# Optimization experiments

Hardware: AMD Instinct MI355X
Metric: run time of the kernel (lower is better)

Reference implementation:

```python
import jax, jax.numpy as jnp
import numpy as np

B = 65536
NEGO = 48        # num_ego_obs
NADO = 24        # num_ado_obs
NTEAMS, TSIZE = 2, 3
NA = NTEAMS * TSIZE          # num_agents = 6
NADOAG = NA - 1              # 5 ado agents
E = 256                      # embed_dims[-1]
H = 4                        # attention heads
AD = 256 // H                # attend_dim = 64


def setup_inputs() -> dict:
    key = jax.random.key(0)
    ks = jax.random.split(key, 16)
    w = lambda k, shape: jax.random.normal(k, shape, jnp.float32) * 0.05
    return {
        "observations": jax.random.normal(ks[0], (B, NEGO + NADOAG * NADO), jnp.float32),
        # ego encoder: Linear(48,256)+LeakyReLU, Linear(256,256)+LeakyReLU
        "ego_w0": w(ks[1], (NEGO, E)), "ego_b0": jnp.zeros((E,), jnp.float32),
        "ego_w1": w(ks[2], (E, E)),    "ego_b1": jnp.zeros((E,), jnp.float32),
        # ado encoder: Linear(25,256)+LeakyReLU, Linear(256,256)+LeakyReLU
        "ado_w0": w(ks[3], (NADO + 1, E)), "ado_b0": jnp.zeros((E,), jnp.float32),
        "ado_w1": w(ks[4], (E, E)),        "ado_b1": jnp.zeros((E,), jnp.float32),
        # per-head extractors stacked on a leading head axis
        "key_w": w(ks[5], (H, E, AD)),   # no bias
        "sel_w": w(ks[6], (H, E, AD)),   # no bias
        "lat_w": w(ks[7], (H, E, AD)), "lat_b": jnp.zeros((H, AD), jnp.float32),
        # projection: Linear(256, 64)
        "proj_w": w(ks[8], (H * AD, AD)), "proj_b": jnp.zeros((AD,), jnp.float32),
    }


def reference(observations, ego_w0, ego_b0, ego_w1, ego_b1,
              ado_w0, ado_b0, ado_w1, ado_b1,
              key_w, sel_w, lat_w, lat_b, proj_w, proj_b):
    lrelu = jax.nn.leaky_relu  # slope 0.01, matches nn.LeakyReLU()
    obs_ego = observations[:, :NEGO]                              # [B, 48]
    obs_ado = observations[:, NEGO:NEGO + NADOAG * NADO]          # [B, 120]
    team_ids = jnp.asarray([t for t in range(NTEAMS) for _ in range(TSIZE)],
                           jnp.float32)                           # [6]

    # ego latent [B, E]
    ego = lrelu(lrelu(obs_ego @ ego_w0 + ego_b0) @ ego_w1 + ego_b1)

    # ado_ag_obs[..., ado_id::5] == reshape(B, NADO, 5)[:, :, ado_id]
    ado_obs = obs_ado.reshape(-1, NADO, NADOAG).transpose(0, 2, 1)  # [B, 5, 24]
    tid = jnp.broadcast_to(team_ids[1:NA][None, :, None],
                           (ado_obs.shape[0], NADOAG, 1))           # [B, 5, 1]
    ado_in = jnp.concatenate([ado_obs, tid], axis=-1)               # [B, 5, 25]
    ado = lrelu(lrelu(ado_in @ ado_w0 + ado_b0) @ ado_w1 + ado_b1)  # [B, 5, E]

    slct = jnp.einsum('be,hed->bhd', ego, sel_w)                    # [B, H, AD]
    keys = jnp.einsum('bne,hed->bnhd', ado, key_w)                  # [B, 5, H, AD]
    lats = lrelu(jnp.einsum('bne,hed->bnhd', ado, lat_w) + lat_b)   # [B, 5, H, AD]

    logits = jnp.einsum('bhd,bnhd->bhn', slct, keys) / jnp.sqrt(jnp.float32(AD))
    attn = jax.nn.softmax(logits, axis=-1)                          # [B, H, 5]
    agg = jnp.einsum('bhn,bnhd->bhd', attn, lats).reshape(-1, H * AD)  # heads concat in order
    proj = agg @ proj_w + proj_b                                    # [B, 64]
    return jnp.concatenate([obs_ego, proj], axis=-1)                # [B, 112]
```

## Files before the change

kernel.cpp:

```cpp
#include <hip/hip_runtime.h>
#include <hip/hip_bf16.h>


typedef __bf16 bf16x8 __attribute__((ext_vector_type(8)));
typedef __bf16 bf16x4 __attribute__((ext_vector_type(4)));
typedef float  f32x4  __attribute__((ext_vector_type(4)));

#define OFF_EGO0 0
#define OFF_EGO1 16384
#define OFF_ADO0 81920
#define OFF_ADO1 90112
#define OFF_SEL  155648
#define OFF_KEY  221184
#define OFF_LAT  286720
#define OFF_PROJ 352256
#define WS_ELEMS 368640

__global__ __launch_bounds__(256) void prep_weights(
    const float* __restrict__ ew0, const float* __restrict__ ew1,
    const float* __restrict__ aw0, const float* __restrict__ aw1,
    const float* __restrict__ keyw, const float* __restrict__ selw,
    const float* __restrict__ latw, const float* __restrict__ projw,
    __bf16* __restrict__ ws)
{
  int i = blockIdx.x * 256 + threadIdx.x;
  if (i >= WS_ELEMS) return;
  float v;
  if (i < OFF_EGO1)      { int j=i;          int c=j>>6, k=j&63;  v = (k<48) ? ew0[k*256+c] : 0.f; }
  else if (i < OFF_ADO0) { int j=i-OFF_EGO1; int c=j>>8, k=j&255; v = ew1[k*256+c]; }
  else if (i < OFF_ADO1) { int j=i-OFF_ADO0; int c=j>>5, k=j&31;  v = (k<25) ? aw0[k*256+c] : 0.f; }
  else if (i < OFF_SEL)  { int j=i-OFF_ADO1; int c=j>>8, k=j&255; v = aw1[k*256+c]; }
  else if (i < OFF_KEY)  { int j=i-OFF_SEL;  int c=j>>8, k=j&255; v = selw[(c>>6)*16384 + k*64 + (c&63)]; }
  else if (i < OFF_LAT)  { int j=i-OFF_KEY;  int c=j>>8, k=j&255; v = keyw[(c>>6)*16384 + k*64 + (c&63)]; }
  else if (i < OFF_PROJ) { int j=i-OFF_LAT;  int c=j>>8, k=j&255; v = latw[(c>>6)*16384 + k*64 + (c&63)]; }
  else                   { int j=i-OFF_PROJ; int c=j>>8, k=j&255; v = projw[k*64+c]; }
  ws[i] = (__bf16)v;
}

__device__ __forceinline__ bf16x8 lds_loadA(const __bf16* base, int row, int kByte, int rowBytes) {
  int off = (row * rowBytes + kByte) ^ ((row & 7) << 4);
  return *reinterpret_cast<const bf16x8*>(reinterpret_cast<const char*>(base) + off);
}
__device__ __forceinline__ void lds_store_bf16(__bf16* base, int row, int col, __bf16 v) {
  int off = (row * 512 + col * 2) ^ ((row & 7) << 4);
  *reinterpret_cast<__bf16*>(reinterpret_cast<char*>(base) + off) = v;
}

#define P_ADO2   0
#define P_EGOIN  0
#define P_EGOH1  2048
#define P_ADOIN  24576
#define P_EGOH2  40960
#define P_PROJIN 40960
#define P_H1     49152
#define P_OUT    73728
#define POOL_BYTES 77824

template<int KP, int R, bool ACT>
__device__ __forceinline__ void gemm_block(const __bf16* __restrict__ sA, int aRow0,
                                           __bf16* __restrict__ sC, int cRow0,
                                           const __bf16* __restrict__ WT,
                                           const float* __restrict__ bias,
                                           int w, int lr, int lg)
{
  constexpr int NKB = KP / 32;
  #pragma unroll
  for (int cth = 0; cth < 2; ++cth) {
    f32x4 acc[R][2];
    #pragma unroll
    for (int t = 0; t < R; ++t) {
      acc[t][0] = f32x4{0.f,0.f,0.f,0.f};
      acc[t][1] = f32x4{0.f,0.f,0.f,0.f};
    }
    #pragma unroll
    for (int kb = 0; kb < NKB; ++kb) {
      bf16x8 af[R];
      #pragma unroll
      for (int t = 0; t < R; ++t)
        af[t] = lds_loadA(sA, aRow0 + t*16 + lr, kb*64 + lg*16, KP*2);
      #pragma unroll
      for (int c2 = 0; c2 < 2; ++c2) {
        const int col = w*64 + (cth*2 + c2)*16 + lr;
        bf16x8 bfr = *reinterpret_cast<const bf16x8*>(WT + col*KP + kb*32 + lg*8);
        #pragma unroll
        for (int t = 0; t < R; ++t)
          acc[t][c2] = __builtin_amdgcn_mfma_f32_16x16x32_bf16(af[t], bfr, acc[t][c2], 0, 0, 0);
      }
    }
    #pragma unroll
    for (int c2 = 0; c2 < 2; ++c2) {
      const int col = w*64 + (cth*2 + c2)*16 + lr;
      const float bv = bias[col];
      #pragma unroll
      for (int t = 0; t < R; ++t) {
        #pragma unroll
        for (int e = 0; e < 4; ++e) {
          float x = acc[t][c2][e] + bv;
          if (ACT) x = x > 0.f ? x : 0.01f * x;
          lds_store_bf16(sC, cRow0 + t*16 + lg*4 + e, col, (__bf16)x);
        }
      }
    }
  }
}

__global__ __launch_bounds__(256) void fused_kernel(
    const float* __restrict__ obs,
    const float* __restrict__ eb0, const float* __restrict__ eb1,
    const float* __restrict__ ab0, const float* __restrict__ ab1,
    const float* __restrict__ latb, const float* __restrict__ projb,
    const __bf16* __restrict__ ws,
    float* __restrict__ out)
{
  const int tid = threadIdx.x;
  const int w  = tid >> 6;
  const int l  = tid & 63;
  const int lr = l & 15;
  const int lg = l >> 4;
  const int b0 = blockIdx.x * 16;

  __shared__ __align__(16) char pool[POOL_BYTES];
  __bf16* sEgoIn = reinterpret_cast<__bf16*>(pool + P_EGOIN);
  __bf16* sEgoH1 = reinterpret_cast<__bf16*>(pool + P_EGOH1);
  __bf16* sAdoIn = reinterpret_cast<__bf16*>(pool + P_ADOIN);
  __bf16* sEgoH2 = reinterpret_cast<__bf16*>(pool + P_EGOH2);
  __bf16* sProj  = reinterpret_cast<__bf16*>(pool + P_PROJIN);
  __bf16* sAdo2  = reinterpret_cast<__bf16*>(pool + P_ADO2);
  __bf16* sH1    = reinterpret_cast<__bf16*>(pool + P_H1);
  float*  sOutF  = reinterpret_cast<float*>(pool + P_OUT);

  {
    if (tid < 192) {
      int row = tid / 12, c4 = tid % 12;
      f32x4 v = *reinterpret_cast<const f32x4*>(obs + (size_t)(b0+row)*168 + c4*4);
      __builtin_nontemporal_store(v,
          reinterpret_cast<f32x4*>(out + (size_t)(b0+row)*112 + c4*4));
      bf16x4 bv = { (__bf16)v[0], (__bf16)v[1], (__bf16)v[2], (__bf16)v[3] };
      int off = (row*128 + c4*8) ^ ((row&7)<<4);
      *reinterpret_cast<bf16x4*>(reinterpret_cast<char*>(sEgoIn) + off) = bv;
    } else {
      int t = tid - 192;
      int row = t >> 2, ch = t & 3;
      bf16x4 z = {};
      int off = (row*128 + 96 + ch*8) ^ ((row&7)<<4);
      *reinterpret_cast<bf16x4*>(reinterpret_cast<char*>(sEgoIn) + off) = z;
    }
    if (tid < 240) {
      int ldsrow = tid / 3, p = tid % 3;
      int n = ldsrow >> 4, r = ldsrow & 15;
      const float* orow = obs + (size_t)(b0+r)*168 + 48;
      bf16x8 v;
      #pragma unroll
      for (int j = 0; j < 8; ++j) v[j] = (__bf16)orow[(p*8+j)*5 + n];
      int off = (ldsrow*64 + p*16) ^ ((ldsrow&7)<<4);
      *reinterpret_cast<bf16x8*>(reinterpret_cast<char*>(sAdoIn) + off) = v;
    }
    if (tid < 80) {
      int n = tid >> 4;
      bf16x8 v = {};
      v[0] = (__bf16)((n >= 2) ? 1.0f : 0.0f);
      int off = (tid*64 + 48) ^ ((tid&7)<<4);
      *reinterpret_cast<bf16x8*>(reinterpret_cast<char*>(sAdoIn) + off) = v;
    }
  }
  __syncthreads();

  gemm_block<64, 1, true>(sEgoIn, 0, sEgoH1, 0, ws + OFF_EGO0, eb0, w, lr, lg);
  gemm_block<32, 3, true>(sAdoIn, 0, sH1,    0, ws + OFF_ADO0, ab0, w, lr, lg);
  __syncthreads();

  gemm_block<256, 1, true>(sEgoH1, 0, sEgoH2, 0, ws + OFF_EGO1, eb1, w, lr, lg);
  __syncthreads();

  f32x4 slct[4];
  {
    const __bf16* WT = ws + OFF_SEL;
    #pragma unroll
    for (int ct = 0; ct < 4; ++ct) slct[ct] = f32x4{0.f,0.f,0.f,0.f};
    #pragma unroll
    for (int kb = 0; kb < 8; ++kb) {
      bf16x8 af = lds_loadA(sEgoH2, lr, kb*64 + lg*16, 512);
      #pragma unroll
      for (int ct = 0; ct < 4; ++ct) {
        bf16x8 bfr = *reinterpret_cast<const bf16x8*>(WT + (w*64+ct*16+lr)*256 + kb*32 + lg*8);
        slct[ct] = __builtin_amdgcn_mfma_f32_16x16x32_bf16(af, bfr, slct[ct], 0, 0, 0);
      }
    }
  }
  gemm_block<256, 3, true>(sH1, 0, sAdo2, 0, ws + OFF_ADO1, ab1, w, lr, lg);
  __syncthreads();

  gemm_block<32, 2, true>(sAdoIn, 48, sH1, 0, ws + OFF_ADO0, ab0, w, lr, lg);
  __syncthreads();

  gemm_block<256, 2, true>(sH1, 0, sAdo2, 48, ws + OFF_ADO1, ab1, w, lr, lg);
  __syncthreads();

  f32x4 part[5];
  #pragma unroll
  for (int n = 0; n < 5; ++n) part[n] = f32x4{0.f,0.f,0.f,0.f};
  {
    const __bf16* WK = ws + OFF_KEY;
    #pragma unroll
    for (int cth = 0; cth < 2; ++cth) {
      f32x4 kacc[5][2];
      #pragma unroll
      for (int n = 0; n < 5; ++n) {
        kacc[n][0] = f32x4{0.f,0.f,0.f,0.f};
        kacc[n][1] = f32x4{0.f,0.f,0.f,0.f};
      }
      #pragma unroll
      for (int kb = 0; kb < 8; ++kb) {
        bf16x8 af[5];
        #pragma unroll
        for (int n = 0; n < 5; ++n)
          af[n] = lds_loadA(sAdo2, n*16 + lr, kb*64 + lg*16, 512);
        #pragma unroll
        for (int c2 = 0; c2 < 2; ++c2) {
          const int col = w*64 + (cth*2 + c2)*16 + lr;
          bf16x8 bk = *reinterpret_cast<const bf16x8*>(WK + col*256 + kb*32 + lg*8);
          #pragma unroll
          for (int n = 0; n < 5; ++n)
            kacc[n][c2] = __builtin_amdgcn_mfma_f32_16x16x32_bf16(af[n], bk, kacc[n][c2], 0, 0, 0);
        }
      }
      #pragma unroll
      for (int c2 = 0; c2 < 2; ++c2)
        #pragma unroll
        for (int n = 0; n < 5; ++n)
          part[n] += kacc[n][c2] * slct[cth*2 + c2];
    }
  }
  #pragma unroll
  for (int n = 0; n < 5; ++n) {
    #pragma unroll
    for (int m = 1; m < 16; m <<= 1) {
      part[n][0] += __shfl_xor(part[n][0], m);
      part[n][1] += __shfl_xor(part[n][1], m);
      part[n][2] += __shfl_xor(part[n][2], m);
      part[n][3] += __shfl_xor(part[n][3], m);
    }
  }
  f32x4 p[5];
  {
    #pragma unroll
    for (int n = 0; n < 5; ++n) part[n] *= 0.125f;
    f32x4 mx = part[0];
    #pragma unroll
    for (int n = 1; n < 5; ++n)
      #pragma unroll
      for (int e = 0; e < 4; ++e) mx[e] = fmaxf(mx[e], part[n][e]);
    f32x4 s = f32x4{0.f,0.f,0.f,0.f};
    #pragma unroll
    for (int n = 0; n < 5; ++n) {
      #pragma unroll
      for (int e = 0; e < 4; ++e) p[n][e] = __expf(part[n][e] - mx[e]);
      s += p[n];
    }
    f32x4 inv;
    #pragma unroll
    for (int e = 0; e < 4; ++e) inv[e] = 1.0f / s[e];
    #pragma unroll
    for (int n = 0; n < 5; ++n) p[n] *= inv;
  }
  f32x4 agg[4];
  #pragma unroll
  for (int ct = 0; ct < 4; ++ct) agg[ct] = f32x4{0.f,0.f,0.f,0.f};
  {
    const __bf16* WL = ws + OFF_LAT;
    #pragma unroll
    for (int cth = 0; cth < 2; ++cth) {
      f32x4 lacc[5][2];
      #pragma unroll
      for (int n = 0; n < 5; ++n) {
        lacc[n][0] = f32x4{0.f,0.f,0.f,0.f};
        lacc[n][1] = f32x4{0.f,0.f,0.f,0.f};
      }
      #pragma unroll
      for (int kb = 0; kb < 8; ++kb) {
        bf16x8 af[5];
        #pragma unroll
        for (int n = 0; n < 5; ++n)
          af[n] = lds_loadA(sAdo2, n*16 + lr, kb*64 + lg*16, 512);
        #pragma unroll
        for (int c2 = 0; c2 < 2; ++c2) {
          const int col = w*64 + (cth*2 + c2)*16 + lr;
          bf16x8 bl = *reinterpret_cast<const bf16x8*>(WL + col*256 + kb*32 + lg*8);
          #pragma unroll
          for (int n = 0; n < 5; ++n)
            lacc[n][c2] = __builtin_amdgcn_mfma_f32_16x16x32_bf16(af[n], bl, lacc[n][c2], 0, 0, 0);
        }
      }
      #pragma unroll
      for (int c2 = 0; c2 < 2; ++c2) {
        const int ct = cth*2 + c2;
        const float lb = latb[w*64 + ct*16 + lr];
        #pragma unroll
        for (int n = 0; n < 5; ++n) {
          #pragma unroll
          for (int e = 0; e < 4; ++e) {
            float x = lacc[n][c2][e] + lb;
            x = x > 0.f ? x : 0.01f * x;
            agg[ct][e] += p[n][e] * x;
          }
        }
      }
    }
  }
  #pragma unroll
  for (int ct = 0; ct < 4; ++ct)
    #pragma unroll
    for (int e = 0; e < 4; ++e)
      lds_store_bf16(sProj, lg*4 + e, w*64 + ct*16 + lr, (__bf16)agg[ct][e]);
  __syncthreads();

  {
    const __bf16* WT = ws + OFF_PROJ;
    f32x4 pacc = f32x4{0.f,0.f,0.f,0.f};
    #pragma unroll
    for (int kb = 0; kb < 8; ++kb) {
      bf16x8 af = lds_loadA(sProj, lr, kb*64 + lg*16, 512);
      bf16x8 bfr = *reinterpret_cast<const bf16x8*>(WT + (w*16+lr)*256 + kb*32 + lg*8);
      pacc = __builtin_amdgcn_mfma_f32_16x16x32_bf16(af, bfr, pacc, 0, 0, 0);
    }
    const float pb = projb[w*16 + lr];
    #pragma unroll
    for (int e = 0; e < 4; ++e)
      sOutF[(lg*4 + e)*64 + w*16 + lr] = pacc[e] + pb;
  }
  __syncthreads();

  {
    int row = tid >> 4, q = tid & 15;
    f32x4 v = *reinterpret_cast<const f32x4*>(sOutF + row*64 + q*4);
    __builtin_nontemporal_store(v,
        reinterpret_cast<f32x4*>(out + (size_t)(b0+row)*112 + 48 + q*4));
  }
}

extern "C" void kernel_launch(void* const* d_in, const int* in_sizes, int n_in,
                              void* d_out, int out_size, void* d_ws, size_t ws_size,
                              hipStream_t stream) {
  const float* obs   = (const float*)d_in[0];
  const float* ew0   = (const float*)d_in[1];
  const float* eb0   = (const float*)d_in[2];
  const float* ew1   = (const float*)d_in[3];
  const float* eb1   = (const float*)d_in[4];
  const float* aw0   = (const float*)d_in[5];
  const float* ab0   = (const float*)d_in[6];
  const float* aw1   = (const float*)d_in[7];
  const float* ab1   = (const float*)d_in[8];
  const float* keyw  = (const float*)d_in[9];
  const float* selw  = (const float*)d_in[10];
  const float* latw  = (const float*)d_in[11];
  const float* latb  = (const float*)d_in[12];
  const float* projw = (const float*)d_in[13];
  const float* projb = (const float*)d_in[14];
  __bf16* ws = (__bf16*)d_ws;
  float* out = (float*)d_out;

  prep_weights<<<dim3((WS_ELEMS + 255)/256), dim3(256), 0, stream>>>(
      ew0, ew1, aw0, aw1, keyw, selw, latw, projw, ws);
  fused_kernel<<<dim3(65536/16), dim3(256), 0, stream>>>(
      obs, eb0, eb1, ab0, ab1, latb, projb, ws, out);
}
```

Measured before the change: 489.1 us.

## Double waves per block, split columns per wave, stage observations in LDS

The fused kernel now launches 512 threads (8 waves) per 16-row tile, and each wave computes 32 output columns instead of 64 in every GEMM stage. Because one attention head now spans two waves, partial logits are exchanged through LDS with an extra barrier before the softmax. Observation rows are first loaded into LDS with coalesced vector loads, replacing the strided global gathers for the ado inputs. The aim is more waves in flight to hide latency and fewer weight fragments per wave. In exchange, every wave still reads all A fragments from LDS, so LDS traffic roughly doubles, and the kernel adds barriers plus idle waves in the final projection and store.

```diff
diff --git a/kernel.cpp b/kernel.cpp
--- a/kernel.cpp
+++ b/kernel.cpp
@@ -53,6 +53,7 @@
 #define P_EGOH2  40960
 #define P_PROJIN 40960
 #define P_H1     49152
+#define P_OBSRAW 49152
 #define P_OUT    73728
 #define POOL_BYTES 77824
 
@@ -64,47 +65,44 @@
                                            int w, int lr, int lg)
 {
   constexpr int NKB = KP / 32;
-  #pragma unroll
-  for (int cth = 0; cth < 2; ++cth) {
-    f32x4 acc[R][2];
+  f32x4 acc[R][2];
+  #pragma unroll
+  for (int t = 0; t < R; ++t) {
+    acc[t][0] = f32x4{0.f,0.f,0.f,0.f};
+    acc[t][1] = f32x4{0.f,0.f,0.f,0.f};
+  }
+  #pragma unroll
+  for (int kb = 0; kb < NKB; ++kb) {
+    bf16x8 af[R];
+    #pragma unroll
+    for (int t = 0; t < R; ++t)
+      af[t] = lds_loadA(sA, aRow0 + t*16 + lr, kb*64 + lg*16, KP*2);
+    #pragma unroll
+    for (int c2 = 0; c2 < 2; ++c2) {
+      const int col = w*32 + c2*16 + lr;
+      bf16x8 bfr = *reinterpret_cast<const bf16x8*>(WT + col*KP + kb*32 + lg*8);
+      #pragma unroll
+      for (int t = 0; t < R; ++t)
+        acc[t][c2] = __builtin_amdgcn_mfma_f32_16x16x32_bf16(af[t], bfr, acc[t][c2], 0, 0, 0);
+    }
+  }
+  #pragma unroll
+  for (int c2 = 0; c2 < 2; ++c2) {
+    const int col = w*32 + c2*16 + lr;
+    const float bv = bias[col];
     #pragma unroll
     for (int t = 0; t < R; ++t) {
-      acc[t][0] = f32x4{0.f,0.f,0.f,0.f};
-      acc[t][1] = f32x4{0.f,0.f,0.f,0.f};
-    }
-    #pragma unroll
-    for (int kb = 0; kb < NKB; ++kb) {
-      bf16x8 af[R];
-      #pragma unroll
-      for (int t = 0; t < R; ++t)
-        af[t] = lds_loadA(sA, aRow0 + t*16 + lr, kb*64 + lg*16, KP*2);
-      #pragma unroll
-      for (int c2 = 0; c2 < 2; ++c2) {
-        const int col = w*64 + (cth*2 + c2)*16 + lr;
-        bf16x8 bfr = *reinterpret_cast<const bf16x8*>(WT + col*KP + kb*32 + lg*8);
-        #pragma unroll
-        for (int t = 0; t < R; ++t)
-          acc[t][c2] = __builtin_amdgcn_mfma_f32_16x16x32_bf16(af[t], bfr, acc[t][c2], 0, 0, 0);
-      }
-    }
-    #pragma unroll
-    for (int c2 = 0; c2 < 2; ++c2) {
-      const int col = w*64 + (cth*2 + c2)*16 + lr;
-      const float bv = bias[col];
-      #pragma unroll
-      for (int t = 0; t < R; ++t) {
-        #pragma unroll
-        for (int e = 0; e < 4; ++e) {
-          float x = acc[t][c2][e] + bv;
-          if (ACT) x = x > 0.f ? x : 0.01f * x;
-          lds_store_bf16(sC, cRow0 + t*16 + lg*4 + e, col, (__bf16)x);
-        }
-      }
-    }
-  }
-}
-
-__global__ __launch_bounds__(256) void fused_kernel(
+      #pragma unroll
+      for (int e = 0; e < 4; ++e) {
+        float x = acc[t][c2][e] + bv;
+        if (ACT) x = x > 0.f ? x : 0.01f * x;
+        lds_store_bf16(sC, cRow0 + t*16 + lg*4 + e, col, (__bf16)x);
+      }
+    }
+  }
+}
+
+__global__ __launch_bounds__(512, 4) void fused_kernel(
     const float* __restrict__ obs,
     const float* __restrict__ eb0, const float* __restrict__ eb1,
     const float* __restrict__ ab0, const float* __restrict__ ab1,
@@ -127,39 +125,55 @@
   __bf16* sProj  = reinterpret_cast<__bf16*>(pool + P_PROJIN);
   __bf16* sAdo2  = reinterpret_cast<__bf16*>(pool + P_ADO2);
   __bf16* sH1    = reinterpret_cast<__bf16*>(pool + P_H1);
+  float*  sObsF  = reinterpret_cast<float*>(pool + P_OBSRAW);
+  float*  sLogF  = reinterpret_cast<float*>(pool + P_OUT);
   float*  sOutF  = reinterpret_cast<float*>(pool + P_OUT);
+
+  {
+    const f32x4* o4 = reinterpret_cast<const f32x4*>(obs);
+    #pragma unroll
+    for (int idx = tid; idx < 672; idx += 512) {
+      int row = idx / 42, c4 = idx % 42;
+      f32x4 v = o4[(size_t)(b0+row)*42 + c4];
+      *reinterpret_cast<f32x4*>(sObsF + row*168 + c4*4) = v;
+      if (c4 < 12)
+        __builtin_nontemporal_store(v,
+            reinterpret_cast<f32x4*>(out + (size_t)(b0+row)*112 + c4*4));
+    }
+  }
+  __syncthreads();
 
   {
     if (tid < 192) {
       int row = tid / 12, c4 = tid % 12;
-      f32x4 v = *reinterpret_cast<const f32x4*>(obs + (size_t)(b0+row)*168 + c4*4);
-      __builtin_nontemporal_store(v,
-          reinterpret_cast<f32x4*>(out + (size_t)(b0+row)*112 + c4*4));
+      f32x4 v = *reinterpret_cast<const f32x4*>(sObsF + row*168 + c4*4);
       bf16x4 bv = { (__bf16)v[0], (__bf16)v[1], (__bf16)v[2], (__bf16)v[3] };
       int off = (row*128 + c4*8) ^ ((row&7)<<4);
       *reinterpret_cast<bf16x4*>(reinterpret_cast<char*>(sEgoIn) + off) = bv;
-    } else {
+    } else if (tid < 256) {
       int t = tid - 192;
       int row = t >> 2, ch = t & 3;
       bf16x4 z = {};
       int off = (row*128 + 96 + ch*8) ^ ((row&7)<<4);
       *reinterpret_cast<bf16x4*>(reinterpret_cast<char*>(sEgoIn) + off) = z;
     }
-    if (tid < 240) {
-      int ldsrow = tid / 3, p = tid % 3;
+    if (tid >= 256 && tid < 496) {
+      int t = tid - 256;
+      int ldsrow = t / 3, p = t % 3;
       int n = ldsrow >> 4, r = ldsrow & 15;
-      const float* orow = obs + (size_t)(b0+r)*168 + 48;
+      const float* orow = sObsF + r*168 + 48;
       bf16x8 v;
       #pragma unroll
       for (int j = 0; j < 8; ++j) v[j] = (__bf16)orow[(p*8+j)*5 + n];
       int off = (ldsrow*64 + p*16) ^ ((ldsrow&7)<<4);
       *reinterpret_cast<bf16x8*>(reinterpret_cast<char*>(sAdoIn) + off) = v;
     }
-    if (tid < 80) {
-      int n = tid >> 4;
+    if (tid >= 432) {
+      int t = tid - 432;
+      int n = t >> 4;
       bf16x8 v = {};
       v[0] = (__bf16)((n >= 2) ? 1.0f : 0.0f);
-      int off = (tid*64 + 48) ^ ((tid&7)<<4);
+      int off = (t*64 + 48) ^ ((t&7)<<4);
       *reinterpret_cast<bf16x8*>(reinterpret_cast<char*>(sAdoIn) + off) = v;
     }
   }
@@ -172,20 +186,22 @@
   gemm_block<256, 1, true>(sEgoH1, 0, sEgoH2, 0, ws + OFF_EGO1, eb1, w, lr, lg);
   __syncthreads();
 
-  f32x4 slct[4];
+  f32x4 slct[2];
   {
     const __bf16* WT = ws + OFF_SEL;
-    #pragma unroll
-    for (int ct = 0; ct < 4; ++ct) slct[ct] = f32x4{0.f,0.f,0.f,0.f};
+    slct[0] = f32x4{0.f,0.f,0.f,0.f};
+    slct[1] = f32x4{0.f,0.f,0.f,0.f};
     #pragma unroll
     for (int kb = 0; kb < 8; ++kb) {
       bf16x8 af = lds_loadA(sEgoH2, lr, kb*64 + lg*16, 512);
       #pragma unroll
-      for (int ct = 0; ct < 4; ++ct) {
-        bf16x8 bfr = *reinterpret_cast<const bf16x8*>(WT + (w*64+ct*16+lr)*256 + kb*32 + lg*8);
-        slct[ct] = __builtin_amdgcn_mfma_f32_16x16x32_bf16(af, bfr, slct[ct], 0, 0, 0);
-      }
-    }
+      for (int c2 = 0; c2 < 2; ++c2) {
+        bf16x8 bfr = *reinterpret_cast<const bf16x8*>(WT + (w*32+c2*16+lr)*256 + kb*32 + lg*8);
+        slct[c2] = __builtin_amdgcn_mfma_f32_16x16x32_bf16(af, bfr, slct[c2], 0, 0, 0);
+      }
+    }
+    slct[0] *= 0.125f;
+    slct[1] *= 0.125f;
   }
   gemm_block<256, 3, true>(sH1, 0, sAdo2, 0, ws + OFF_ADO1, ab1, w, lr, lg);
   __syncthreads();
@@ -202,33 +218,24 @@
   {
     const __bf16* WK = ws + OFF_KEY;
     #pragma unroll
-    for (int cth = 0; cth < 2; ++cth) {
-      f32x4 kacc[5][2];
-      #pragma unroll
-      for (int n = 0; n < 5; ++n) {
-        kacc[n][0] = f32x4{0.f,0.f,0.f,0.f};
-        kacc[n][1] = f32x4{0.f,0.f,0.f,0.f};
-      }
+    for (int c2 = 0; c2 < 2; ++c2) {
+      f32x4 kacc[5];
+      #pragma unroll
+      for (int n = 0; n < 5; ++n) kacc[n] = f32x4{0.f,0.f,0.f,0.f};
+      const int col = w*32 + c2*16 + lr;
       #pragma unroll
       for (int kb = 0; kb < 8; ++kb) {
         bf16x8 af[5];
         #pragma unroll
         for (int n = 0; n < 5; ++n)
           af[n] = lds_loadA(sAdo2, n*16 + lr, kb*64 + lg*16, 512);
-        #pragma unroll
-        for (int c2 = 0; c2 < 2; ++c2) {
-          const int col = w*64 + (cth*2 + c2)*16 + lr;
-          bf16x8 bk = *reinterpret_cast<const bf16x8*>(WK + col*256 + kb*32 + lg*8);
-          #pragma unroll
-          for (int n = 0; n < 5; ++n)
-            kacc[n][c2] = __builtin_amdgcn_mfma_f32_16x16x32_bf16(af[n], bk, kacc[n][c2], 0, 0, 0);
-        }
-      }
-      #pragma unroll
-      for (int c2 = 0; c2 < 2; ++c2)
+        bf16x8 bk = *reinterpret_cast<const bf16x8*>(WK + col*256 + kb*32 + lg*8);
         #pragma unroll
         for (int n = 0; n < 5; ++n)
-          part[n] += kacc[n][c2] * slct[cth*2 + c2];
+          kacc[n] = __builtin_amdgcn_mfma_f32_16x16x32_bf16(af[n], bk, kacc[n], 0, 0, 0);
+      }
+      #pragma unroll
+      for (int n = 0; n < 5; ++n) part[n] += kacc[n] * slct[c2];
     }
   }
   #pragma unroll
@@ -241,20 +248,28 @@
       part[n][3] += __shfl_xor(part[n][3], m);
     }
   }
+  #pragma unroll
+  for (int n = 0; n < 5; ++n)
+    if (lr == n)
+      *reinterpret_cast<f32x4*>(sLogF + (w*5 + n)*16 + lg*4) = part[n];
+  __syncthreads();
   f32x4 p[5];
   {
-    #pragma unroll
-    for (int n = 0; n < 5; ++n) part[n] *= 0.125f;
-    f32x4 mx = part[0];
+    f32x4 lt[5];
+    #pragma unroll
+    for (int n = 0; n < 5; ++n)
+      lt[n] = *reinterpret_cast<const f32x4*>(sLogF + (w*5 + n)*16 + lg*4)
+            + *reinterpret_cast<const f32x4*>(sLogF + ((w^1)*5 + n)*16 + lg*4);
+    f32x4 mx = lt[0];
     #pragma unroll
     for (int n = 1; n < 5; ++n)
       #pragma unroll
-      for (int e = 0; e < 4; ++e) mx[e] = fmaxf(mx[e], part[n][e]);
+      for (int e = 0; e < 4; ++e) mx[e] = fmaxf(mx[e], lt[n][e]);
     f32x4 s = f32x4{0.f,0.f,0.f,0.f};
     #pragma unroll
     for (int n = 0; n < 5; ++n) {
       #pragma unroll
-      for (int e = 0; e < 4; ++e) p[n][e] = __expf(part[n][e] - mx[e]);
+      for (int e = 0; e < 4; ++e) p[n][e] = __expf(lt[n][e] - mx[e]);
       s += p[n];
     }
     f32x4 inv;
@@ -263,58 +278,48 @@
     #pragma unroll
     for (int n = 0; n < 5; ++n) p[n] *= inv;
   }
-  f32x4 agg[4];
-  #pragma unroll
-  for (int ct = 0; ct < 4; ++ct) agg[ct] = f32x4{0.f,0.f,0.f,0.f};
+  f32x4 agg[2];
+  agg[0] = f32x4{0.f,0.f,0.f,0.f};
+  agg[1] = f32x4{0.f,0.f,0.f,0.f};
   {
     const __bf16* WL = ws + OFF_LAT;
     #pragma unroll
-    for (int cth = 0; cth < 2; ++cth) {
-      f32x4 lacc[5][2];
-      #pragma unroll
-      for (int n = 0; n < 5; ++n) {
-        lacc[n][0] = f32x4{0.f,0.f,0.f,0.f};
-        lacc[n][1] = f32x4{0.f,0.f,0.f,0.f};
-      }
+    for (int c2 = 0; c2 < 2; ++c2) {
+      f32x4 lacc[5];
+      #pragma unroll
+      for (int n = 0; n < 5; ++n) lacc[n] = f32x4{0.f,0.f,0.f,0.f};
+      const int col = w*32 + c2*16 + lr;
       #pragma unroll
       for (int kb = 0; kb < 8; ++kb) {
         bf16x8 af[5];
         #pragma unroll
         for (int n = 0; n < 5; ++n)
           af[n] = lds_loadA(sAdo2, n*16 + lr, kb*64 + lg*16, 512);
-        #pragma unroll
-        for (int c2 = 0; c2 < 2; ++c2) {
-          const int col = w*64 + (cth*2 + c2)*16 + lr;
-          bf16x8 bl = *reinterpret_cast<const bf16x8*>(WL + col*256 + kb*32 + lg*8);
-          #pragma unroll
-          for (int n = 0; n < 5; ++n)
-            lacc[n][c2] = __builtin_amdgcn_mfma_f32_16x16x32_bf16(af[n], bl, lacc[n][c2], 0, 0, 0);
+        bf16x8 bl = *reinterpret_cast<const bf16x8*>(WL + col*256 + kb*32 + lg*8);
+        #pragma unroll
+        for (int n = 0; n < 5; ++n)
+          lacc[n] = __builtin_amdgcn_mfma_f32_16x16x32_bf16(af[n], bl, lacc[n], 0, 0, 0);
+      }
+      const float lb = latb[col];
+      #pragma unroll
+      for (int n = 0; n < 5; ++n) {
+        #pragma unroll
+        for (int e = 0; e < 4; ++e) {
+          float x = lacc[n][e] + lb;
+          x = x > 0.f ? x : 0.01f * x;
+          agg[c2][e] += p[n][e] * x;
         }
       }
-      #pragma unroll
-      for (int c2 = 0; c2 < 2; ++c2) {
-        const int ct = cth*2 + c2;
-        const float lb = latb[w*64 + ct*16 + lr];
-        #pragma unroll
-        for (int n = 0; n < 5; ++n) {
-          #pragma unroll
-          for (int e = 0; e < 4; ++e) {
-            float x = lacc[n][c2][e] + lb;
-            x = x > 0.f ? x : 0.01f * x;
-            agg[ct][e] += p[n][e] * x;
-          }
-        }
-      }
-    }
-  }
-  #pragma unroll
-  for (int ct = 0; ct < 4; ++ct)
+    }
+  }
+  #pragma unroll
+  for (int c2 = 0; c2 < 2; ++c2)
     #pragma unroll
     for (int e = 0; e < 4; ++e)
-      lds_store_bf16(sProj, lg*4 + e, w*64 + ct*16 + lr, (__bf16)agg[ct][e]);
-  __syncthreads();
-
-  {
+      lds_store_bf16(sProj, lg*4 + e, w*32 + c2*16 + lr, (__bf16)agg[c2][e]);
+  __syncthreads();
+
+  if (w < 4) {
     const __bf16* WT = ws + OFF_PROJ;
     f32x4 pacc = f32x4{0.f,0.f,0.f,0.f};
     #pragma unroll
@@ -330,7 +335,7 @@
   }
   __syncthreads();
 
-  {
+  if (tid < 256) {
     int row = tid >> 4, q = tid & 15;
     f32x4 v = *reinterpret_cast<const f32x4*>(sOutF + row*64 + q*4);
     __builtin_nontemporal_store(v,
@@ -361,6 +366,6 @@
 
   prep_weights<<<dim3((WS_ELEMS + 255)/256), dim3(256), 0, stream>>>(
       ew0, ew1, aw0, aw1, keyw, selw, latw, projw, ws);
-  fused_kernel<<<dim3(65536/16), dim3(256), 0, stream>>>(
+  fused_kernel<<<dim3(65536/16), dim3(512), 0, stream>>>(
       obs, eb0, eb1, ab0, ab1, latb, projb, ws, out);
 }
```

New measurement: 457.7 us. 1.07x faster.

## Shrink LDS pool with in-place ado GEMMs to raise occupancy

Applied to the files above, without the earlier changes.

Reorganizes shared-memory use so the second ado layer runs in place over its input, with a barrier between the accumulate and writeback phases, which cuts the LDS pool from about 76KB to 40KB. It also sets launch_bounds to 4 blocks per CU, stages the raw observation tile into LDS with coalesced vector loads instead of strided global gathers, and folds the 1/sqrt(d) scale into the selector. The gemm helper now keeps four column tiles of accumulators live, which raises register pressure, and it adds extra block-wide barriers.

```diff
diff --git a/kernel.cpp b/kernel.cpp
--- a/kernel.cpp
+++ b/kernel.cpp
@@ -46,65 +46,61 @@
   *reinterpret_cast<__bf16*>(reinterpret_cast<char*>(base) + off) = v;
 }
 
-#define P_ADO2   0
 #define P_EGOIN  0
 #define P_EGOH1  2048
-#define P_ADOIN  24576
-#define P_EGOH2  40960
-#define P_PROJIN 40960
-#define P_H1     49152
-#define P_OUT    73728
-#define POOL_BYTES 77824
-
-template<int KP, int R, bool ACT>
-__device__ __forceinline__ void gemm_block(const __bf16* __restrict__ sA, int aRow0,
-                                           __bf16* __restrict__ sC, int cRow0,
-                                           const __bf16* __restrict__ WT,
-                                           const float* __restrict__ bias,
-                                           int w, int lr, int lg)
+#define P_OBSRAW 10752
+#define P_EGOH2  21504
+#define P_ADOIN  29696
+#define P_PROJIN 0
+#define P_OUTF   8192
+#define POOL_BYTES 40960
+
+template<int KP, int R, bool SYNCW>
+__device__ __forceinline__ void gemm4(const __bf16* __restrict__ sA, int aRow0,
+                                      __bf16* __restrict__ sC, int cRow0,
+                                      const __bf16* __restrict__ WT,
+                                      const float* __restrict__ bias,
+                                      int w, int lr, int lg)
 {
   constexpr int NKB = KP / 32;
-  #pragma unroll
-  for (int cth = 0; cth < 2; ++cth) {
-    f32x4 acc[R][2];
+  f32x4 acc[R][4];
+  #pragma unroll
+  for (int t = 0; t < R; ++t)
+    #pragma unroll
+    for (int ct = 0; ct < 4; ++ct) acc[t][ct] = f32x4{0.f,0.f,0.f,0.f};
+  #pragma unroll
+  for (int kb = 0; kb < NKB; ++kb) {
+    bf16x8 af[R];
+    #pragma unroll
+    for (int t = 0; t < R; ++t)
+      af[t] = lds_loadA(sA, aRow0 + t*16 + lr, kb*64 + lg*16, KP*2);
+    #pragma unroll
+    for (int ct = 0; ct < 4; ++ct) {
+      const int col = w*64 + ct*16 + lr;
+      bf16x8 bfr = *reinterpret_cast<const bf16x8*>(WT + col*KP + kb*32 + lg*8);
+      #pragma unroll
+      for (int t = 0; t < R; ++t)
+        acc[t][ct] = __builtin_amdgcn_mfma_f32_16x16x32_bf16(af[t], bfr, acc[t][ct], 0, 0, 0);
+    }
+  }
+  if (SYNCW) __syncthreads();
+  #pragma unroll
+  for (int ct = 0; ct < 4; ++ct) {
+    const int col = w*64 + ct*16 + lr;
+    const float bv = bias[col];
     #pragma unroll
     for (int t = 0; t < R; ++t) {
-      acc[t][0] = f32x4{0.f,0.f,0.f,0.f};
-      acc[t][1] = f32x4{0.f,0.f,0.f,0.f};
-    }
-    #pragma unroll
-    for (int kb = 0; kb < NKB; ++kb) {
-      bf16x8 af[R];
-      #pragma unroll
-      for (int t = 0; t < R; ++t)
-        af[t] = lds_loadA(sA, aRow0 + t*16 + lr, kb*64 + lg*16, KP*2);
-      #pragma unroll
-      for (int c2 = 0; c2 < 2; ++c2) {
-        const int col = w*64 + (cth*2 + c2)*16 + lr;
-        bf16x8 bfr = *reinterpret_cast<const bf16x8*>(WT + col*KP + kb*32 + lg*8);
-        #pragma unroll
-        for (int t = 0; t < R; ++t)
-          acc[t][c2] = __builtin_amdgcn_mfma_f32_16x16x32_bf16(af[t], bfr, acc[t][c2], 0, 0, 0);
-      }
-    }
-    #pragma unroll
-    for (int c2 = 0; c2 < 2; ++c2) {
-      const int col = w*64 + (cth*2 + c2)*16 + lr;
-      const float bv = bias[col];
-      #pragma unroll
-      for (int t = 0; t < R; ++t) {
-        #pragma unroll
-        for (int e = 0; e < 4; ++e) {
-          float x = acc[t][c2][e] + bv;
-          if (ACT) x = x > 0.f ? x : 0.01f * x;
-          lds_store_bf16(sC, cRow0 + t*16 + lg*4 + e, col, (__bf16)x);
-        }
-      }
-    }
-  }
-}
-
-__global__ __launch_bounds__(256) void fused_kernel(
+      #pragma unroll
+      for (int e = 0; e < 4; ++e) {
+        float x = acc[t][ct][e] + bv;
+        x = x > 0.f ? x : 0.01f * x;
+        lds_store_bf16(sC, cRow0 + t*16 + lg*4 + e, col, (__bf16)x);
+      }
+    }
+  }
+}
+
+__global__ __launch_bounds__(256, 4) void fused_kernel(
     const float* __restrict__ obs,
     const float* __restrict__ eb0, const float* __restrict__ eb1,
     const float* __restrict__ ab0, const float* __restrict__ ab1,
@@ -122,19 +118,30 @@
   __shared__ __align__(16) char pool[POOL_BYTES];
   __bf16* sEgoIn = reinterpret_cast<__bf16*>(pool + P_EGOIN);
   __bf16* sEgoH1 = reinterpret_cast<__bf16*>(pool + P_EGOH1);
+  __bf16* sEgoH2 = reinterpret_cast<__bf16*>(pool + P_EGOH2);
   __bf16* sAdoIn = reinterpret_cast<__bf16*>(pool + P_ADOIN);
-  __bf16* sEgoH2 = reinterpret_cast<__bf16*>(pool + P_EGOH2);
+  __bf16* sAdo2  = reinterpret_cast<__bf16*>(pool);
   __bf16* sProj  = reinterpret_cast<__bf16*>(pool + P_PROJIN);
-  __bf16* sAdo2  = reinterpret_cast<__bf16*>(pool + P_ADO2);
-  __bf16* sH1    = reinterpret_cast<__bf16*>(pool + P_H1);
-  float*  sOutF  = reinterpret_cast<float*>(pool + P_OUT);
+  float*  sObsF  = reinterpret_cast<float*>(pool + P_OBSRAW);
+  float*  sOutF  = reinterpret_cast<float*>(pool + P_OUTF);
+
+  {
+    const f32x4* o4 = reinterpret_cast<const f32x4*>(obs);
+    for (int idx = tid; idx < 672; idx += 256) {
+      int row = idx / 42, c4 = idx % 42;
+      f32x4 v = o4[(size_t)(b0+row)*42 + c4];
+      *reinterpret_cast<f32x4*>(sObsF + row*168 + c4*4) = v;
+      if (c4 < 12)
+        __builtin_nontemporal_store(v,
+            reinterpret_cast<f32x4*>(out + (size_t)(b0+row)*112 + c4*4));
+    }
+  }
+  __syncthreads();
 
   {
     if (tid < 192) {
       int row = tid / 12, c4 = tid % 12;
-      f32x4 v = *reinterpret_cast<const f32x4*>(obs + (size_t)(b0+row)*168 + c4*4);
-      __builtin_nontemporal_store(v,
-          reinterpret_cast<f32x4*>(out + (size_t)(b0+row)*112 + c4*4));
+      f32x4 v = *reinterpret_cast<const f32x4*>(sObsF + row*168 + c4*4);
       bf16x4 bv = { (__bf16)v[0], (__bf16)v[1], (__bf16)v[2], (__bf16)v[3] };
       int off = (row*128 + c4*8) ^ ((row&7)<<4);
       *reinterpret_cast<bf16x4*>(reinterpret_cast<char*>(sEgoIn) + off) = bv;
@@ -148,7 +155,7 @@
     if (tid < 240) {
       int ldsrow = tid / 3, p = tid % 3;
       int n = ldsrow >> 4, r = ldsrow & 15;
-      const float* orow = obs + (size_t)(b0+r)*168 + 48;
+      const float* orow = sObsF + r*168 + 48;
       bf16x8 v;
       #pragma unroll
       for (int j = 0; j < 8; ++j) v[j] = (__bf16)orow[(p*8+j)*5 + n];
@@ -165,35 +172,101 @@
   }
   __syncthreads();
 
-  gemm_block<64, 1, true>(sEgoIn, 0, sEgoH1, 0, ws + OFF_EGO0, eb0, w, lr, lg);
-  gemm_block<32, 3, true>(sAdoIn, 0, sH1,    0, ws + OFF_ADO0, ab0, w, lr, lg);
-  __syncthreads();
-
-  gemm_block<256, 1, true>(sEgoH1, 0, sEgoH2, 0, ws + OFF_EGO1, eb1, w, lr, lg);
+  gemm4<64, 1, false>(sEgoIn, 0, sEgoH1, 0, ws + OFF_EGO0, eb0, w, lr, lg);
+  __syncthreads();
+
+  gemm4<256, 1, false>(sEgoH1, 0, sEgoH2, 0, ws + OFF_EGO1, eb1, w, lr, lg);
   __syncthreads();
 
   f32x4 slct[4];
   {
     const __bf16* WT = ws + OFF_SEL;
     #pragma unroll
-    for (int ct = 0; ct < 4; ++ct) slct[ct] = f32x4{0.f,0.f,0.f,0.f};
-    #pragma unroll
-    for (int kb = 0; kb < 8; ++kb) {
-      bf16x8 af = lds_loadA(sEgoH2, lr, kb*64 + lg*16, 512);
-      #pragma unroll
-      for (int ct = 0; ct < 4; ++ct) {
-        bf16x8 bfr = *reinterpret_cast<const bf16x8*>(WT + (w*64+ct*16+lr)*256 + kb*32 + lg*8);
-        slct[ct] = __builtin_amdgcn_mfma_f32_16x16x32_bf16(af, bfr, slct[ct], 0, 0, 0);
-      }
-    }
-  }
-  gemm_block<256, 3, true>(sH1, 0, sAdo2, 0, ws + OFF_ADO1, ab1, w, lr, lg);
-  __syncthreads();
-
-  gemm_block<32, 2, true>(sAdoIn, 48, sH1, 0, ws + OFF_ADO0, ab0, w, lr, lg);
-  __syncthreads();
-
-  gemm_block<256, 2, true>(sH1, 0, sAdo2, 48, ws + OFF_ADO1, ab1, w, lr, lg);
+    for (int pair = 0; pair < 2; ++pair) {
+      f32x4 sacc[2];
+      sacc[0] = f32x4{0.f,0.f,0.f,0.f};
+      sacc[1] = f32x4{0.f,0.f,0.f,0.f};
+      #pragma unroll
+      for (int kb = 0; kb < 8; ++kb) {
+        bf16x8 af = lds_loadA(sEgoH2, lr, kb*64 + lg*16, 512);
+        #pragma unroll
+        for (int c2 = 0; c2 < 2; ++c2) {
+          const int col = w*64 + (pair*2 + c2)*16 + lr;
+          bf16x8 bfr = *reinterpret_cast<const bf16x8*>(WT + col*256 + kb*32 + lg*8);
+          sacc[c2] = __builtin_amdgcn_mfma_f32_16x16x32_bf16(af, bfr, sacc[c2], 0, 0, 0);
+        }
+      }
+      slct[pair*2 + 0] = sacc[0] * 0.125f;
+      slct[pair*2 + 1] = sacc[1] * 0.125f;
+    }
+  }
+  __syncthreads();
+
+  {
+    const __bf16* WT = ws + OFF_ADO0;
+    bf16x8 af[5];
+    #pragma unroll
+    for (int n = 0; n < 5; ++n)
+      af[n] = lds_loadA(sAdoIn, n*16 + lr, lg*16, 64);
+    f32x4 acc[5][2];
+    #pragma unroll
+    for (int n = 0; n < 5; ++n) {
+      acc[n][0] = f32x4{0.f,0.f,0.f,0.f};
+      acc[n][1] = f32x4{0.f,0.f,0.f,0.f};
+    }
+    #pragma unroll
+    for (int c2 = 0; c2 < 2; ++c2) {
+      const int col = w*64 + c2*16 + lr;
+      bf16x8 bfr = *reinterpret_cast<const bf16x8*>(WT + col*32 + lg*8);
+      #pragma unroll
+      for (int n = 0; n < 5; ++n)
+        acc[n][c2] = __builtin_amdgcn_mfma_f32_16x16x32_bf16(af[n], bfr, acc[n][c2], 0, 0, 0);
+    }
+    __syncthreads();
+    #pragma unroll
+    for (int c2 = 0; c2 < 2; ++c2) {
+      const int col = w*64 + c2*16 + lr;
+      const float bv = ab0[col];
+      #pragma unroll
+      for (int n = 0; n < 5; ++n)
+        #pragma unroll
+        for (int e = 0; e < 4; ++e) {
+          float x = acc[n][c2][e] + bv;
+          x = x > 0.f ? x : 0.01f * x;
+          lds_store_bf16(sAdo2, n*16 + lg*4 + e, col, (__bf16)x);
+        }
+    }
+    #pragma unroll
+    for (int n = 0; n < 5; ++n) {
+      acc[n][0] = f32x4{0.f,0.f,0.f,0.f};
+      acc[n][1] = f32x4{0.f,0.f,0.f,0.f};
+    }
+    #pragma unroll
+    for (int c2 = 0; c2 < 2; ++c2) {
+      const int col = w*64 + (2 + c2)*16 + lr;
+      bf16x8 bfr = *reinterpret_cast<const bf16x8*>(WT + col*32 + lg*8);
+      #pragma unroll
+      for (int n = 0; n < 5; ++n)
+        acc[n][c2] = __builtin_amdgcn_mfma_f32_16x16x32_bf16(af[n], bfr, acc[n][c2], 0, 0, 0);
+    }
+    #pragma unroll
+    for (int c2 = 0; c2 < 2; ++c2) {
+      const int col = w*64 + (2 + c2)*16 + lr;
+      const float bv = ab0[col];
+      #pragma unroll
+      for (int n = 0; n < 5; ++n)
+        #pragma unroll
+        for (int e = 0; e < 4; ++e) {
+          float x = acc[n][c2][e] + bv;
+          x = x > 0.f ? x : 0.01f * x;
+          lds_store_bf16(sAdo2, n*16 + lg*4 + e, col, (__bf16)x);
+        }
+    }
+  }
+  __syncthreads();
+
+  gemm4<256, 3, true>(sAdo2, 0,  sAdo2, 0,  ws + OFF_ADO1, ab1, w, lr, lg);
+  gemm4<256, 2, true>(sAdo2, 48, sAdo2, 48, ws + OFF_ADO1, ab1, w, lr, lg);
   __syncthreads();
 
   f32x4 part[5];
@@ -202,7 +275,7 @@
   {
     const __bf16* WK = ws + OFF_KEY;
     #pragma unroll
-    for (int cth = 0; cth < 2; ++cth) {
+    for (int pair = 0; pair < 2; ++pair) {
       f32x4 kacc[5][2];
       #pragma unroll
       for (int n = 0; n < 5; ++n) {
@@ -217,7 +290,7 @@
           af[n] = lds_loadA(sAdo2, n*16 + lr, kb*64 + lg*16, 512);
         #pragma unroll
         for (int c2 = 0; c2 < 2; ++c2) {
-          const int col = w*64 + (cth*2 + c2)*16 + lr;
+          const int col = w*64 + (pair*2 + c2)*16 + lr;
           bf16x8 bk = *reinterpret_cast<const bf16x8*>(WK + col*256 + kb*32 + lg*8);
           #pragma unroll
           for (int n = 0; n < 5; ++n)
@@ -225,10 +298,8 @@
         }
       }
       #pragma unroll
-      for (int c2 = 0; c2 < 2; ++c2)
-        #pragma unroll
-        for (int n = 0; n < 5; ++n)
-          part[n] += kacc[n][c2] * slct[cth*2 + c2];
+      for (int n = 0; n < 5; ++n)
+        part[n] += kacc[n][0]*slct[pair*2] + kacc[n][1]*slct[pair*2+1];
     }
   }
   #pragma unroll
@@ -243,8 +314,6 @@
   }
   f32x4 p[5];
   {
-    #pragma unroll
-    for (int n = 0; n < 5; ++n) part[n] *= 0.125f;
     f32x4 mx = part[0];
     #pragma unroll
     for (int n = 1; n < 5; ++n)
@@ -269,7 +338,7 @@
   {
     const __bf16* WL = ws + OFF_LAT;
     #pragma unroll
-    for (int cth = 0; cth < 2; ++cth) {
+    for (int pair = 0; pair < 2; ++pair) {
       f32x4 lacc[5][2];
       #pragma unroll
       for (int n = 0; n < 5; ++n) {
@@ -284,7 +353,7 @@
           af[n] = lds_loadA(sAdo2, n*16 + lr, kb*64 + lg*16, 512);
         #pragma unroll
         for (int c2 = 0; c2 < 2; ++c2) {
-          const int col = w*64 + (cth*2 + c2)*16 + lr;
+          const int col = w*64 + (pair*2 + c2)*16 + lr;
           bf16x8 bl = *reinterpret_cast<const bf16x8*>(WL + col*256 + kb*32 + lg*8);
           #pragma unroll
           for (int n = 0; n < 5; ++n)
@@ -293,20 +362,20 @@
       }
       #pragma unroll
       for (int c2 = 0; c2 < 2; ++c2) {
-        const int ct = cth*2 + c2;
+        const int ct = pair*2 + c2;
         const float lb = latb[w*64 + ct*16 + lr];
         #pragma unroll
-        for (int n = 0; n < 5; ++n) {
+        for (int n = 0; n < 5; ++n)
           #pragma unroll
           for (int e = 0; e < 4; ++e) {
             float x = lacc[n][c2][e] + lb;
             x = x > 0.f ? x : 0.01f * x;
             agg[ct][e] += p[n][e] * x;
           }
-        }
-      }
-    }
-  }
+      }
+    }
+  }
+  __syncthreads();
   #pragma unroll
   for (int ct = 0; ct < 4; ++ct)
     #pragma unroll
```

Result: slower. 1.510 ms (+208.7%).
